# Kernel tuning notes

Hardware: AMD Instinct MI355X
Metric: run time of the kernel (lower is better)

Reference implementation:

```python
import jax, jax.numpy as jnp
import numpy as np

N = 50000
E = 800000
D = 128
NUM_GRAPHS = 64
NEG_SLOPE = 0.2


def _gat_conv(x, src, dst, W, a_src, a_dst, bias):
    """PyG GATConv with heads=1, concat=True. src/dst include self-loops."""
    h = x @ W                                  # [N, D_out]
    alpha_s = h @ a_src                        # [N]
    alpha_d = h @ a_dst                        # [N]
    e = alpha_s[src] + alpha_d[dst]            # [E_tot] edge scores
    e = jnp.where(e > 0, e, NEG_SLOPE * e)     # LeakyReLU(0.2)
    # numerically-stable softmax over incoming edges of each dst node
    m = jax.ops.segment_max(e, dst, num_segments=N)
    m = jnp.where(jnp.isfinite(m), m, 0.0)
    ex = jnp.exp(e - m[dst])
    s = jax.ops.segment_sum(ex, dst, num_segments=N)
    coef = ex / (s[dst] + 1e-16)               # [E_tot]
    msg = h[src] * coef[:, None]               # [E_tot, D_out] gathered messages
    out = jax.ops.segment_sum(msg, dst, num_segments=N)
    return out + bias


def setup_inputs() -> dict:
    key = jax.random.key(0)
    ks = jax.random.split(key, 12)
    x = jax.random.normal(ks[0], (N, D), dtype=jnp.float32)
    edge_index = jax.random.randint(ks[1], (2, E), 0, N, dtype=jnp.int64)
    batch = jnp.sort(jax.random.randint(ks[2], (N,), 0, NUM_GRAPHS, dtype=jnp.int64))
    g = 1.0 / np.sqrt(D)
    W1 = jax.random.normal(ks[3], (D, D), dtype=jnp.float32) * g
    as1 = jax.random.normal(ks[4], (D,), dtype=jnp.float32) * g
    ad1 = jax.random.normal(ks[5], (D,), dtype=jnp.float32) * g
    b1 = jnp.zeros((D,), dtype=jnp.float32)
    W2 = jax.random.normal(ks[6], (D, D), dtype=jnp.float32) * g
    as2 = jax.random.normal(ks[7], (D,), dtype=jnp.float32) * g
    ad2 = jax.random.normal(ks[8], (D,), dtype=jnp.float32) * g
    b2 = jnp.zeros((D,), dtype=jnp.float32)
    return {"x": x, "edge_index": edge_index, "batch": batch,
            "W1": W1, "as1": as1, "ad1": ad1, "b1": b1,
            "W2": W2, "as2": as2, "ad2": ad2, "b2": b2}


def reference(x, edge_index, batch, W1, as1, ad1, b1, W2, as2, ad2, b2):
    # PyG GATConv adds self-loops by default
    loops = jnp.arange(N, dtype=edge_index.dtype)
    src = jnp.concatenate([edge_index[0], loops])
    dst = jnp.concatenate([edge_index[1], loops])
    feats = _gat_conv(x, src, dst, W1, as1, ad1, b1)
    feats = _gat_conv(feats, src, dst, W2, as2, ad2, b2)
    # global mean pool over graphs in the batch
    sums = jax.ops.segment_sum(feats, batch, num_segments=NUM_GRAPHS)
    counts = jax.ops.segment_sum(jnp.ones((N,), feats.dtype), batch, num_segments=NUM_GRAPHS)
    pooled = sums / jnp.maximum(counts, 1.0)[:, None]
    return feats, pooled
```

## Files before the change

### kernel.cpp

```cpp
#include <hip/hip_runtime.h>

#define NN 50000
#define NE 800000
#define DIM 128
#define NG 64
#define ETOT (NE + NN)
#define NEG_SLOPE 0.2f
#define PB 200
#define MAXLG 8
#define NSH 8
#define SHW ((NN + NSH - 1) / NSH)
#define NB_SCAN ((NN + 255) / 256)

typedef unsigned int uint32;
typedef unsigned short ushort;
typedef short bf16x8 __attribute__((ext_vector_type(8)));
typedef float f32x4 __attribute__((ext_vector_type(4)));

static __device__ __forceinline__ uint32 f2bf_pack(float lo, float hi) {
  uint32 a = __float_as_uint(lo), b = __float_as_uint(hi);
  a = (a + 0x7fffu + ((a >> 16) & 1u)) >> 16;
  b = (b + 0x7fffu + ((b >> 16) & 1u)) >> 16;
  return a | (b << 16);
}
static __device__ __forceinline__ ushort f2bf1(float x) {
  uint32 a = __float_as_uint(x);
  a = (a + 0x7fffu + ((a >> 16) & 1u)) >> 16;
  return (ushort)a;
}
static __device__ __forceinline__ float bf_lo(uint32 u) { return __uint_as_float(u << 16); }
static __device__ __forceinline__ float bf_hi(uint32 u) { return __uint_as_float(u & 0xffff0000u); }


__global__ __launch_bounds__(256) void k_init(int* deg, int* fill, float* pooled, float* cnt) {
  int i = blockIdx.x * 256 + threadIdx.x;
  if (i < NN) { deg[i] = 1; fill[i] = 1; }
  if (i < NG * DIM) pooled[i] = 0.f;
  if (i < NG) cnt[i] = 0.f;
}

__global__ __launch_bounds__(256) void k_prep(const float* __restrict__ W1, const float* __restrict__ W2,
                                              ushort* __restrict__ wt1, ushort* __restrict__ wt2) {
  int i = blockIdx.x * 256 + threadIdx.x;
  if (i < DIM * DIM) {
    int n = i >> 7, k = i & 127;
    wt1[i] = f2bf1(W1[k * DIM + n]);
    wt2[i] = f2bf1(W2[k * DIM + n]);
  }
}

__global__ __launch_bounds__(256) void k_count(const int* __restrict__ dst, int* __restrict__ deg) {
  int e = blockIdx.x * 256 + threadIdx.x;
  if (e < NE) atomicAdd(&deg[dst[e]], 1);
}


__global__ __launch_bounds__(256) void k_scan1(const int* __restrict__ deg, int* __restrict__ offs,
                                               int* __restrict__ bsum) {
  __shared__ int ws[4];
  const int i = blockIdx.x * 256 + threadIdx.x;
  const int lane = threadIdx.x & 63, wid = threadIdx.x >> 6;
  int x = (i < NN) ? deg[i] : 0;
#pragma unroll
  for (int off = 1; off < 64; off <<= 1) {
    int t = __shfl_up(x, off, 64);
    if (lane >= off) x += t;
  }
  if (lane == 63) ws[wid] = x;
  __syncthreads();
  int pre = 0;
#pragma unroll
  for (int j = 0; j < 3; ++j) if (j < wid) pre += ws[j];
  x += pre;
  if (i < NN) offs[i + 1] = x;
  if (threadIdx.x == 255) bsum[blockIdx.x] = x;
}

__global__ __launch_bounds__(256) void k_scan2(const int* __restrict__ bsum, int* __restrict__ bpre) {
  __shared__ int ws[4];
  const int b = threadIdx.x;
  const int lane = b & 63, wid = b >> 6;
  int v = (b < NB_SCAN) ? bsum[b] : 0;
  int x = v;
#pragma unroll
  for (int off = 1; off < 64; off <<= 1) {
    int t = __shfl_up(x, off, 64);
    if (lane >= off) x += t;
  }
  if (lane == 63) ws[wid] = x;
  __syncthreads();
  int pre = 0;
#pragma unroll
  for (int j = 0; j < 3; ++j) if (j < wid) pre += ws[j];
  x += pre;
  if (b < NB_SCAN) bpre[b] = x - v;
}

__global__ __launch_bounds__(256) void k_scan3(int* __restrict__ offs, const int* __restrict__ bpre) {
  const int i = blockIdx.x * 256 + threadIdx.x;
  if (i < NN) offs[i + 1] += bpre[blockIdx.x];
  if (i == 0) offs[0] = 0;
}

__global__ __launch_bounds__(256) void k_selfloop(const int* __restrict__ offs, int* __restrict__ csr) {
  int i = blockIdx.x * 256 + threadIdx.x;
  if (i < NN) csr[offs[i]] = i;
}

__global__ __launch_bounds__(256) void k_scatter(const int* __restrict__ src, const int* __restrict__ dst,
                                                 const int* __restrict__ offs, int* __restrict__ fill,
                                                 int* __restrict__ csr) {
  const int r = blockIdx.x & (NSH - 1);
  const int bi = blockIdx.x >> 3;
  const int nb = gridDim.x >> 3;
  const int lo = r * SHW, hi = min(lo + SHW, NN);
  for (int e = bi * 256 + threadIdx.x; e < NE; e += nb * 256) {
    int d = dst[e];
    if (d >= lo && d < hi) {
      int p = offs[d] + atomicAdd(&fill[d], 1);
      csr[p] = src[e];
    }
  }
}


template <int A16>
__global__ __launch_bounds__(256) void k_mm(const void* __restrict__ Xv, const ushort* __restrict__ WT,
                                            const float* __restrict__ a_s, const float* __restrict__ a_d,
                                            uint32* __restrict__ H16,
                                            float* __restrict__ alpha_s, float* __restrict__ alpha_d, int n) {
  __shared__ __align__(16) ushort sWT[DIM * DIM];
  __shared__ __align__(16) ushort sA[64 * DIM];
  const int tid = threadIdx.x;
  const int row0 = blockIdx.x * 64;

  {
    const int nr = tid >> 1, h2 = tid & 1;
    const uint4* wp = (const uint4*)(WT + nr * DIM + h2 * 64);
#pragma unroll
    for (int i = 0; i < 8; ++i) {
      uint4 v = wp[i];
      int byte = nr * 256 + (((h2 * 128 + i * 16)) ^ ((nr & 7) << 4));
      *(uint4*)((char*)sWT + byte) = v;
    }
  }
  {
    const int r = tid >> 2, q = tid & 3;
    int rg = row0 + r; if (rg > n - 1) rg = n - 1;
    if (A16) {
      const uint4* xp = (const uint4*)((const uint32*)Xv + (size_t)rg * 64 + q * 16);
#pragma unroll
      for (int i = 0; i < 4; ++i) {
        uint4 pk = xp[i];
        int byte = r * 256 + ((q * 64 + i * 16) ^ ((r & 7) << 4));
        *(uint4*)((char*)sA + byte) = pk;
      }
    } else {
      const float4* xp = (const float4*)((const float*)Xv + (size_t)rg * DIM + q * 32);
#pragma unroll
      for (int i = 0; i < 4; ++i) {
        float4 v0 = xp[2 * i], v1 = xp[2 * i + 1];
        uint4 pk = make_uint4(f2bf_pack(v0.x, v0.y), f2bf_pack(v0.z, v0.w),
                              f2bf_pack(v1.x, v1.y), f2bf_pack(v1.z, v1.w));
        int byte = r * 256 + ((q * 64 + i * 16) ^ ((r & 7) << 4));
        *(uint4*)((char*)sA + byte) = pk;
      }
    }
  }
  __syncthreads();

  const int l = tid & 63, wv = tid >> 6;
  const int jr = l & 15, g = l >> 4;
  const int m0 = wv * 16;
  f32x4 acc[8];
#pragma unroll
  for (int nt = 0; nt < 8; ++nt) acc[nt] = (f32x4){0.f, 0.f, 0.f, 0.f};

  const int ra = m0 + jr;
  const int abase = ra * 256, aswz = (ra & 7) << 4;
  const int bswz = (jr & 7) << 4;
#pragma unroll
  for (int kk = 0; kk < 4; ++kk) {
    const int kb = kk * 64 + g * 16;
    bf16x8 af = *(const bf16x8*)((const char*)sA + abase + (kb ^ aswz));
#pragma unroll
    for (int nt = 0; nt < 8; ++nt) {
      bf16x8 bfg = *(const bf16x8*)((const char*)sWT + (nt * 16 + jr) * 256 + (kb ^ bswz));
      acc[nt] = __builtin_amdgcn_mfma_f32_16x16x32_bf16(af, bfg, acc[nt], 0, 0, 0);
    }
  }

  float asv[8], adv[8];
#pragma unroll
  for (int nt = 0; nt < 8; ++nt) { asv[nt] = a_s[nt * 16 + jr]; adv[nt] = a_d[nt * 16 + jr]; }
#pragma unroll
  for (int j = 0; j < 4; ++j) {
    float ps = 0.f, pd = 0.f;
#pragma unroll
    for (int nt = 0; nt < 8; ++nt) {
      ps = fmaf(acc[nt][j], asv[nt], ps);
      pd = fmaf(acc[nt][j], adv[nt], pd);
    }
#pragma unroll
    for (int off = 1; off < 16; off <<= 1) {
      ps += __shfl_xor(ps, off, 64);
      pd += __shfl_xor(pd, off, 64);
    }
    int r = row0 + m0 + g * 4 + j;
    if (jr == 0 && r < n) { alpha_s[r] = ps; alpha_d[r] = pd; }
  }

  ushort* sOut = sA;
#pragma unroll
  for (int nt = 0; nt < 8; ++nt)
#pragma unroll
    for (int j = 0; j < 4; ++j)
      sOut[(m0 + g * 4 + j) * DIM + nt * 16 + jr] = f2bf1(acc[nt][j]);
#pragma unroll
  for (int i = 0; i < 4; ++i) {
    int r = row0 + m0 + (l >> 4) + i * 4;
    uint4 v = *(const uint4*)((const char*)sOut + m0 * 256 + l * 16 + i * 1024);
    if (r < n) *(uint4*)(H16 + (size_t)(row0 + m0) * 64 + l * 4 + i * 256) = v;
  }
}


#define AGGR4(J)                                                        \
  { int s0 = __shfl(sv, (J), 64), s1 = __shfl(sv, (J) + 1, 64),         \
        s2 = __shfl(sv, (J) + 2, 64), s3 = __shfl(sv, (J) + 3, 64);     \
    float c0 = __shfl(ex, (J), 64), c1 = __shfl(ex, (J) + 1, 64),       \
          c2 = __shfl(ex, (J) + 2, 64), c3 = __shfl(ex, (J) + 3, 64);   \
    uint32 u0 = H16[(size_t)s0 * 64 + l];                               \
    uint32 u1 = H16[(size_t)s1 * 64 + l];                               \
    uint32 u2 = H16[(size_t)s2 * 64 + l];                               \
    uint32 u3 = H16[(size_t)s3 * 64 + l];                               \
    ax = fmaf(c0, bf_lo(u0), ax); ay = fmaf(c0, bf_hi(u0), ay);         \
    ax = fmaf(c1, bf_lo(u1), ax); ay = fmaf(c1, bf_hi(u1), ay);         \
    ax = fmaf(c2, bf_lo(u2), ax); ay = fmaf(c2, bf_hi(u2), ay);         \
    ax = fmaf(c3, bf_lo(u3), ax); ay = fmaf(c3, bf_hi(u3), ay); }

#define AGGR1(J)                                                        \
  { int s0 = __shfl(sv, (J), 64); float c0 = __shfl(ex, (J), 64);       \
    uint32 u0 = H16[(size_t)s0 * 64 + l];                               \
    ax = fmaf(c0, bf_lo(u0), ax); ay = fmaf(c0, bf_hi(u0), ay); }

template <int STORE16>
__global__ __launch_bounds__(256) void k_sm_aggr(const int* __restrict__ offs, const int* __restrict__ csr,
                                                 const float* __restrict__ alpha_s, const float* __restrict__ alpha_d,
                                                 const uint32* __restrict__ H16, const float* __restrict__ bias,
                                                 float* __restrict__ out, uint32* __restrict__ out16) {
  const int wave = (blockIdx.x * 256 + threadIdx.x) >> 6;
  const int l = threadIdx.x & 63;
  if (wave >= NN) return;
  const int beg = offs[wave], end = offs[wave + 1];
  const int deg = end - beg;
  const float ad = alpha_d[wave];
  float ax = 0.f, ay = 0.f, ssum = 0.f;

  if (deg <= 64) {
    int sv = 0; float sc = -1e30f;
    if (l < deg) {
      sv = csr[beg + l];
      sc = alpha_s[sv] + ad;
      sc = sc > 0.f ? sc : NEG_SLOPE * sc;
    }
    float m = sc;
#pragma unroll
    for (int off = 1; off < 64; off <<= 1) m = fmaxf(m, __shfl_xor(m, off, 64));
    float ex = (l < deg) ? __expf(sc - m) : 0.f;
    ssum = ex;
    int j = 0;
    for (; j + 3 < deg; j += 4) AGGR4(j);
    for (; j < deg; ++j) AGGR1(j);
  } else {
    float m = -1e30f;
    for (int b = beg + l; b < end; b += 64) {
      float sc = alpha_s[csr[b]] + ad;
      sc = sc > 0.f ? sc : NEG_SLOPE * sc;
      m = fmaxf(m, sc);
    }
#pragma unroll
    for (int off = 1; off < 64; off <<= 1) m = fmaxf(m, __shfl_xor(m, off, 64));
    for (int base = beg; base < end; base += 64) {
      int nch = min(64, end - base);
      int sv = 0; float ex = 0.f;
      if (l < nch) {
        sv = csr[base + l];
        float sc = alpha_s[sv] + ad;
        sc = sc > 0.f ? sc : NEG_SLOPE * sc;
        ex = __expf(sc - m);
      }
      ssum += ex;
      int j = 0;
      for (; j + 3 < nch; j += 4) AGGR4(j);
      for (; j < nch; ++j) AGGR1(j);
    }
  }

#pragma unroll
  for (int off = 1; off < 64; off <<= 1) ssum += __shfl_xor(ssum, off, 64);
  const float inv = 1.f / (ssum + 1e-16f);
  float2 b = *(const float2*)(bias + 2 * l);
  float ox = ax * inv + b.x, oy = ay * inv + b.y;
  if (STORE16) {
    out16[(size_t)wave * 64 + l] = f2bf_pack(ox, oy);
  } else {
    *(float2*)(out + (size_t)wave * DIM + 2 * l) = make_float2(ox, oy);
  }
}


__global__ __launch_bounds__(256) void k_pool_partial(const float* __restrict__ feats,
                                                      const int* __restrict__ batch,
                                                      float* __restrict__ pooled, float* __restrict__ cnt) {
  __shared__ float acc[4][MAXLG][DIM];
  __shared__ float lcnt[4][MAXLG];
  const int tid = threadIdx.x;
  const int wid = tid >> 6, l = tid & 63;
  for (int i = tid; i < 4 * MAXLG * DIM; i += 256) ((float*)acc)[i] = 0.f;
  if (tid < 4 * MAXLG) ((float*)lcnt)[tid] = 0.f;
  __syncthreads();

  const int chunk = (NN + PB - 1) / PB;
  const int beg = blockIdx.x * chunk;
  const int end = min(beg + chunk, NN);
  const int g0 = (beg < NN) ? batch[beg] : 0;

  for (int node = beg + wid; node < end; node += 4) {
    int lg = batch[node] - g0;
    float2 v = *(const float2*)(feats + (size_t)node * DIM + 2 * l);
    if (lg < MAXLG) {
      acc[wid][lg][2 * l] += v.x;
      acc[wid][lg][2 * l + 1] += v.y;
      if (l == 0) lcnt[wid][lg] += 1.f;
    } else {
      atomicAdd(&pooled[(g0 + lg) * DIM + 2 * l], v.x);
      atomicAdd(&pooled[(g0 + lg) * DIM + 2 * l + 1], v.y);
      if (l == 0) atomicAdd(&cnt[g0 + lg], 1.f);
    }
  }
  __syncthreads();

  for (int i = tid; i < MAXLG * DIM; i += 256) {
    int lg = i >> 7, d = i & (DIM - 1);
    float s = acc[0][lg][d] + acc[1][lg][d] + acc[2][lg][d] + acc[3][lg][d];
    if (s != 0.f) atomicAdd(&pooled[(g0 + lg) * DIM + d], s);
  }
  if (tid < MAXLG) {
    float s = lcnt[0][tid] + lcnt[1][tid] + lcnt[2][tid] + lcnt[3][tid];
    if (s != 0.f) atomicAdd(&cnt[g0 + tid], s);
  }
}

__global__ __launch_bounds__(256) void k_pool_norm(float* pooled, const float* __restrict__ cnt) {
  int i = blockIdx.x * 256 + threadIdx.x;
  if (i < NG * DIM) pooled[i] /= fmaxf(cnt[i >> 7], 1.f);
}


static inline size_t pad256(size_t x) { return (x + 255) & ~(size_t)255; }

extern "C" void kernel_launch(void* const* d_in, const int* in_sizes, int n_in,
                              void* d_out, int out_size, void* d_ws, size_t ws_size,
                              hipStream_t stream) {
  const float* x   = (const float*)d_in[0];
  const int* ei    = (const int*)d_in[1];
  const int* batch = (const int*)d_in[2];
  const float* W1  = (const float*)d_in[3];
  const float* as1 = (const float*)d_in[4];
  const float* ad1 = (const float*)d_in[5];
  const float* b1  = (const float*)d_in[6];
  const float* W2  = (const float*)d_in[7];
  const float* as2 = (const float*)d_in[8];
  const float* ad2 = (const float*)d_in[9];
  const float* b2  = (const float*)d_in[10];

  float* out_feats = (float*)d_out;
  float* pooled    = out_feats + (size_t)NN * DIM;

  const int* src = ei;
  const int* dst = ei + NE;

  char* w = (char*)d_ws;
  uint32* h16 = (uint32*)w;   w += pad256((size_t)NN * 64 * 4);
  uint32* f116 = (uint32*)w;  w += pad256((size_t)NN * 64 * 4);
  float* alpha_s = (float*)w; w += pad256((size_t)NN * 4);
  float* alpha_d = (float*)w; w += pad256((size_t)NN * 4);
  int* deg  = (int*)w;        w += pad256((size_t)NN * 4);
  int* offs = (int*)w;        w += pad256((size_t)(NN + 1) * 4);
  int* fill = (int*)w;        w += pad256((size_t)NN * 4);
  int* csr  = (int*)w;        w += pad256((size_t)ETOT * 4);
  float* cnt  = (float*)w;    w += pad256((size_t)NG * 4);
  int* bsum = (int*)w;        w += pad256((size_t)NB_SCAN * 4);
  int* bpre = (int*)w;        w += pad256((size_t)NB_SCAN * 4);
  ushort* wt1 = (ushort*)w;   w += pad256((size_t)DIM * DIM * 2);
  ushort* wt2 = (ushort*)w;   w += pad256((size_t)DIM * DIM * 2);

  const int NB_N = (NN + 255) / 256;
  const int NB_E = (NE + 255) / 256;
  const int NB_W = (NN * 64 + 255) / 256;
  const int NB_G = (NN + 63) / 64;
  const int NB_SC = 1024;

  k_init<<<NB_N, 256, 0, stream>>>(deg, fill, pooled, cnt);
  k_prep<<<(DIM * DIM + 255) / 256, 256, 0, stream>>>(W1, W2, wt1, wt2);
  k_count<<<NB_E, 256, 0, stream>>>(dst, deg);
  k_scan1<<<NB_SCAN, 256, 0, stream>>>(deg, offs, bsum);
  k_scan2<<<1, 256, 0, stream>>>(bsum, bpre);
  k_scan3<<<NB_SCAN, 256, 0, stream>>>(offs, bpre);
  k_selfloop<<<NB_N, 256, 0, stream>>>(offs, csr);
  k_scatter<<<NB_SC, 256, 0, stream>>>(src, dst, offs, fill, csr);

  k_mm<0><<<NB_G, 256, 0, stream>>>(x, wt1, as1, ad1, h16, alpha_s, alpha_d, NN);
  k_sm_aggr<1><<<NB_W, 256, 0, stream>>>(offs, csr, alpha_s, alpha_d, h16, b1, nullptr, f116);

  k_mm<1><<<NB_G, 256, 0, stream>>>(f116, wt2, as2, ad2, h16, alpha_s, alpha_d, NN);
  k_sm_aggr<0><<<NB_W, 256, 0, stream>>>(offs, csr, alpha_s, alpha_d, h16, b2, out_feats, nullptr);

  k_pool_partial<<<PB, 256, 0, stream>>>(out_feats, batch, pooled, cnt);
  k_pool_norm<<<(NG * DIM + 255) / 256, 256, 0, stream>>>(pooled, cnt);
}
```

Measured before the change: 222.9 us.

## Split aggregation waves into half-waves covering two nodes and half the features

The softmax-aggregate kernel now maps each 64-lane wave to two destination nodes, one per 32-lane half, and each block covers half the 128 feature columns. Node pairs are therefore processed twice, once per feature half, and the gather loop runs to the larger degree of the two nodes in a wave. This is meant to improve lane utilisation for the typical in-degree of about 17, which left most of a 64-lane wave idle in the score phase. It also folds the weight-transpose kernel into the init kernel to save a launch. The cost is duplicated score and softmax work per feature half, and divergence when the two paired nodes have different degrees.

```diff
diff --git a/kernel.cpp b/kernel.cpp
--- a/kernel.cpp
+++ b/kernel.cpp
@@ -32,16 +32,13 @@
 static __device__ __forceinline__ float bf_hi(uint32 u) { return __uint_as_float(u & 0xffff0000u); }
 
 
-__global__ __launch_bounds__(256) void k_init(int* deg, int* fill, float* pooled, float* cnt) {
+__global__ __launch_bounds__(256) void k_init(const float* __restrict__ W1, const float* __restrict__ W2,
+                                              ushort* __restrict__ wt1, ushort* __restrict__ wt2,
+                                              int* deg, int* fill, float* pooled, float* cnt) {
   int i = blockIdx.x * 256 + threadIdx.x;
   if (i < NN) { deg[i] = 1; fill[i] = 1; }
   if (i < NG * DIM) pooled[i] = 0.f;
   if (i < NG) cnt[i] = 0.f;
-}
-
-__global__ __launch_bounds__(256) void k_prep(const float* __restrict__ W1, const float* __restrict__ W2,
-                                              ushort* __restrict__ wt1, ushort* __restrict__ wt2) {
-  int i = blockIdx.x * 256 + threadIdx.x;
   if (i < DIM * DIM) {
     int n = i >> 7, k = i & 127;
     wt1[i] = f2bf1(W1[k * DIM + n]);
@@ -225,87 +222,95 @@
 }
 
 
-#define AGGR4(J)                                                        \
-  { int s0 = __shfl(sv, (J), 64), s1 = __shfl(sv, (J) + 1, 64),         \
-        s2 = __shfl(sv, (J) + 2, 64), s3 = __shfl(sv, (J) + 3, 64);     \
-    float c0 = __shfl(ex, (J), 64), c1 = __shfl(ex, (J) + 1, 64),       \
-          c2 = __shfl(ex, (J) + 2, 64), c3 = __shfl(ex, (J) + 3, 64);   \
-    uint32 u0 = H16[(size_t)s0 * 64 + l];                               \
-    uint32 u1 = H16[(size_t)s1 * 64 + l];                               \
-    uint32 u2 = H16[(size_t)s2 * 64 + l];                               \
-    uint32 u3 = H16[(size_t)s3 * 64 + l];                               \
-    ax = fmaf(c0, bf_lo(u0), ax); ay = fmaf(c0, bf_hi(u0), ay);         \
-    ax = fmaf(c1, bf_lo(u1), ax); ay = fmaf(c1, bf_hi(u1), ay);         \
-    ax = fmaf(c2, bf_lo(u2), ax); ay = fmaf(c2, bf_hi(u2), ay);         \
-    ax = fmaf(c3, bf_lo(u3), ax); ay = fmaf(c3, bf_hi(u3), ay); }
-
-#define AGGR1(J)                                                        \
-  { int s0 = __shfl(sv, (J), 64); float c0 = __shfl(ex, (J), 64);       \
-    uint32 u0 = H16[(size_t)s0 * 64 + l];                               \
-    ax = fmaf(c0, bf_lo(u0), ax); ay = fmaf(c0, bf_hi(u0), ay); }
+#define GATHER4(J)                                                          \
+  { int s0 = __shfl(sv, g32 + (J), 64), s1 = __shfl(sv, g32 + (J) + 1, 64), \
+        s2 = __shfl(sv, g32 + (J) + 2, 64), s3 = __shfl(sv, g32 + (J) + 3, 64); \
+    float c0 = __shfl(ex, g32 + (J), 64), c1 = __shfl(ex, g32 + (J) + 1, 64), \
+          c2 = __shfl(ex, g32 + (J) + 2, 64), c3 = __shfl(ex, g32 + (J) + 3, 64); \
+    uint32 v0 = H16[(size_t)s0 * 64 + u0];                                  \
+    uint32 v1 = H16[(size_t)s1 * 64 + u0];                                  \
+    uint32 v2 = H16[(size_t)s2 * 64 + u0];                                  \
+    uint32 v3 = H16[(size_t)s3 * 64 + u0];                                  \
+    ax = fmaf(c0, bf_lo(v0), ax); ay = fmaf(c0, bf_hi(v0), ay);             \
+    ax = fmaf(c1, bf_lo(v1), ax); ay = fmaf(c1, bf_hi(v1), ay);             \
+    ax = fmaf(c2, bf_lo(v2), ax); ay = fmaf(c2, bf_hi(v2), ay);             \
+    ax = fmaf(c3, bf_lo(v3), ax); ay = fmaf(c3, bf_hi(v3), ay); }
+
+#define GATHER1(J)                                                          \
+  { int s0 = __shfl(sv, g32 + (J), 64); float c0 = __shfl(ex, g32 + (J), 64); \
+    uint32 v0 = H16[(size_t)s0 * 64 + u0];                                  \
+    ax = fmaf(c0, bf_lo(v0), ax); ay = fmaf(c0, bf_hi(v0), ay); }
 
 template <int STORE16>
-__global__ __launch_bounds__(256) void k_sm_aggr(const int* __restrict__ offs, const int* __restrict__ csr,
-                                                 const float* __restrict__ alpha_s, const float* __restrict__ alpha_d,
-                                                 const uint32* __restrict__ H16, const float* __restrict__ bias,
-                                                 float* __restrict__ out, uint32* __restrict__ out16) {
-  const int wave = (blockIdx.x * 256 + threadIdx.x) >> 6;
+__global__ __launch_bounds__(256) void k_sm_aggr2(const int* __restrict__ offs, const int* __restrict__ csr,
+                                                  const float* __restrict__ alpha_s, const float* __restrict__ alpha_d,
+                                                  const uint32* __restrict__ H16, const float* __restrict__ bias,
+                                                  float* __restrict__ out, uint32* __restrict__ out16) {
+  const int b = blockIdx.x;
+  const int half = b & 1;
   const int l = threadIdx.x & 63;
-  if (wave >= NN) return;
-  const int beg = offs[wave], end = offs[wave + 1];
-  const int deg = end - beg;
-  const float ad = alpha_d[wave];
+  const int sl = l & 31, g = l >> 5, g32 = g * 32;
+  const int pair = (b >> 1) * 4 + (threadIdx.x >> 6);
+  const int node = pair * 2 + g;
+  const int bg = offs[node], eg = offs[node + 1];
+  const int dg = eg - bg;
+  const float ad = alpha_d[node];
+  const int u0 = half * 32 + sl;
+
+  const int maxd = max(dg, __shfl_xor(dg, 32, 64));
   float ax = 0.f, ay = 0.f, ssum = 0.f;
 
-  if (deg <= 64) {
+  if (maxd <= 32) {
     int sv = 0; float sc = -1e30f;
-    if (l < deg) {
-      sv = csr[beg + l];
+    if (sl < dg) {
+      sv = csr[bg + sl];
       sc = alpha_s[sv] + ad;
       sc = sc > 0.f ? sc : NEG_SLOPE * sc;
     }
     float m = sc;
 #pragma unroll
-    for (int off = 1; off < 64; off <<= 1) m = fmaxf(m, __shfl_xor(m, off, 64));
-    float ex = (l < deg) ? __expf(sc - m) : 0.f;
+    for (int off = 1; off < 32; off <<= 1) m = fmaxf(m, __shfl_xor(m, off, 64));
+    float ex = (sl < dg) ? __expf(sc - m) : 0.f;
     ssum = ex;
     int j = 0;
-    for (; j + 3 < deg; j += 4) AGGR4(j);
-    for (; j < deg; ++j) AGGR1(j);
+    for (; j + 3 < maxd; j += 4) GATHER4(j);
+    for (; j < maxd; ++j) GATHER1(j);
   } else {
     float m = -1e30f;
-    for (int b = beg + l; b < end; b += 64) {
-      float sc = alpha_s[csr[b]] + ad;
+    for (int j = sl; j < dg; j += 32) {
+      float sc = alpha_s[csr[bg + j]] + ad;
       sc = sc > 0.f ? sc : NEG_SLOPE * sc;
       m = fmaxf(m, sc);
     }
 #pragma unroll
-    for (int off = 1; off < 64; off <<= 1) m = fmaxf(m, __shfl_xor(m, off, 64));
-    for (int base = beg; base < end; base += 64) {
-      int nch = min(64, end - base);
+    for (int off = 1; off < 32; off <<= 1) m = fmaxf(m, __shfl_xor(m, off, 64));
+    const int nch = (maxd + 31) >> 5;
+    for (int c = 0; c < nch; ++c) {
+      int j = c * 32 + sl;
       int sv = 0; float ex = 0.f;
-      if (l < nch) {
-        sv = csr[base + l];
+      if (j < dg) {
+        sv = csr[bg + j];
         float sc = alpha_s[sv] + ad;
         sc = sc > 0.f ? sc : NEG_SLOPE * sc;
         ex = __expf(sc - m);
       }
       ssum += ex;
-      int j = 0;
-      for (; j + 3 < nch; j += 4) AGGR4(j);
-      for (; j < nch; ++j) AGGR1(j);
-    }
-  }
-
-#pragma unroll
-  for (int off = 1; off < 64; off <<= 1) ssum += __shfl_xor(ssum, off, 64);
+      int cnt = min(32, maxd - c * 32);
+      int jj = 0;
+      for (; jj + 3 < cnt; jj += 4) GATHER4(jj);
+      for (; jj < cnt; ++jj) GATHER1(jj);
+    }
+  }
+
+#pragma unroll
+  for (int off = 1; off < 32; off <<= 1) ssum += __shfl_xor(ssum, off, 64);
   const float inv = 1.f / (ssum + 1e-16f);
-  float2 b = *(const float2*)(bias + 2 * l);
-  float ox = ax * inv + b.x, oy = ay * inv + b.y;
+  const float2 bb = *(const float2*)(bias + 2 * u0);
+  const float ox = ax * inv + bb.x, oy = ay * inv + bb.y;
   if (STORE16) {
-    out16[(size_t)wave * 64 + l] = f2bf_pack(ox, oy);
+    out16[(size_t)node * 64 + u0] = f2bf_pack(ox, oy);
   } else {
-    *(float2*)(out + (size_t)wave * DIM + 2 * l) = make_float2(ox, oy);
+    *(float2*)(out + (size_t)node * DIM + 2 * u0) = make_float2(ox, oy);
   }
 }
 
@@ -398,12 +403,11 @@
 
   const int NB_N = (NN + 255) / 256;
   const int NB_E = (NE + 255) / 256;
-  const int NB_W = (NN * 64 + 255) / 256;
+  const int NB_A = (NN / 2 / 4) * 2;
   const int NB_G = (NN + 63) / 64;
   const int NB_SC = 1024;
 
-  k_init<<<NB_N, 256, 0, stream>>>(deg, fill, pooled, cnt);
-  k_prep<<<(DIM * DIM + 255) / 256, 256, 0, stream>>>(W1, W2, wt1, wt2);
+  k_init<<<NB_N, 256, 0, stream>>>(W1, W2, wt1, wt2, deg, fill, pooled, cnt);
   k_count<<<NB_E, 256, 0, stream>>>(dst, deg);
   k_scan1<<<NB_SCAN, 256, 0, stream>>>(deg, offs, bsum);
   k_scan2<<<1, 256, 0, stream>>>(bsum, bpre);
@@ -412,10 +416,10 @@
   k_scatter<<<NB_SC, 256, 0, stream>>>(src, dst, offs, fill, csr);
 
   k_mm<0><<<NB_G, 256, 0, stream>>>(x, wt1, as1, ad1, h16, alpha_s, alpha_d, NN);
-  k_sm_aggr<1><<<NB_W, 256, 0, stream>>>(offs, csr, alpha_s, alpha_d, h16, b1, nullptr, f116);
+  k_sm_aggr2<1><<<NB_A, 256, 0, stream>>>(offs, csr, alpha_s, alpha_d, h16, b1, nullptr, f116);
 
   k_mm<1><<<NB_G, 256, 0, stream>>>(f116, wt2, as2, ad2, h16, alpha_s, alpha_d, NN);
-  k_sm_aggr<0><<<NB_W, 256, 0, stream>>>(offs, csr, alpha_s, alpha_d, h16, b2, out_feats, nullptr);
+  k_sm_aggr2<0><<<NB_A, 256, 0, stream>>>(offs, csr, alpha_s, alpha_d, h16, b2, out_feats, nullptr);
 
   k_pool_partial<<<PB, 256, 0, stream>>>(out_feats, batch, pooled, cnt);
   k_pool_norm<<<(NG * DIM + 255) / 256, 256, 0, stream>>>(pooled, cnt);
```

Result: no change. 220.3 us (-1.2%).
